# Performance work log

Measured on AMD Instinct MI355X. Metric: run time of the kernel, lower is better.

The kernel has to match this reference:

```python
import jax, jax.numpy as jnp
import numpy as np

C = 128
K = 7
RED = 4
C_RED = C // RED
PAD = (K - 1) // 2
BN_EPS = 1e-5


def setup_inputs() -> dict:
    key = jax.random.key(0)
    ks = jax.random.split(key, 7)
    b, h, w = 8, 56, 56
    x = jax.random.normal(ks[0], (b, C, h, w), dtype=jnp.float32)
    # 1x1 conv #1: c -> c_red
    w1 = jax.random.normal(ks[1], (C_RED, C), dtype=jnp.float32) * (1.0 / np.sqrt(C))
    b1 = jax.random.normal(ks[2], (C_RED,), dtype=jnp.float32) * 0.01
    # BatchNorm affine params
    gamma = jnp.ones((C_RED,), dtype=jnp.float32)
    beta = jnp.zeros((C_RED,), dtype=jnp.float32)
    # 1x1 conv #2: c_red -> k*k
    w2 = jax.random.normal(ks[3], (K * K, C_RED), dtype=jnp.float32) * (1.0 / np.sqrt(C_RED))
    b2 = jax.random.normal(ks[4], (K * K,), dtype=jnp.float32) * 0.01
    return {"x": x, "w1": w1, "b1": b1, "gamma": gamma, "beta": beta, "w2": w2, "b2": b2}


def _unfold(x):
    # torch.nn.Unfold(K, padding=PAD, stride=1) -> (b, c, k*k, h, w), channel-major
    b, c, h, w = x.shape
    xp = jnp.pad(x, ((0, 0), (0, 0), (PAD, PAD), (PAD, PAD)))
    patches = [xp[:, :, i:i + h, j:j + w] for i in range(K) for j in range(K)]
    return jnp.stack(patches, axis=2)  # (b, c, k*k, h, w)


def reference(x, w1, b1, gamma, beta, w2, b2):
    b, c, h, w = x.shape
    # kernel-generation branch: 1x1 conv -> BN (batch stats, training mode) -> ReLU -> 1x1 conv
    t = jnp.einsum('rc,bchw->brhw', w1, x) + b1[None, :, None, None]
    mean = t.mean(axis=(0, 2, 3))
    var = t.var(axis=(0, 2, 3))  # biased, as in torch BN normalization
    t = (t - mean[None, :, None, None]) * jax.lax.rsqrt(var + BN_EPS)[None, :, None, None]
    t = jax.nn.relu(t * gamma[None, :, None, None] + beta[None, :, None, None])
    kern = jnp.einsum('kr,brhw->bkhw', w2, t) + b2[None, :, None, None]  # (b, k*k, h, w)
    # involution: per-pixel kernel broadcast over channels, sum over k*k taps
    x_unf = _unfold(x)  # (b, c, k*k, h, w)
    return jnp.einsum('bkhw,bckhw->bchw', kern, x_unf)
```

## Files before the change

### kernel.cpp

```cpp
#include <hip/hip_runtime.h>

#define C 128
#define CRED 32
#define K 7
#define KK 49
#define H 56
#define W 56
#define P (H*W)
#define B 8
#define NPIX (B*P)
#define BN_EPS 1e-5

#define T_OFF 0
#define T_SIZE (B*CRED*P)
#define KERN_OFF (T_OFF + T_SIZE)
#define KERN_SIZE (B*KK*P)
#define NBLK_A (49*B)
#define PSUM_OFF (KERN_OFF + KERN_SIZE)
#define PSQ_OFF (PSUM_OFF + NBLK_A*CRED)
#define SS_OFF  (PSQ_OFF + NBLK_A*CRED)
#define SCALE_OFF SS_OFF
#define SHIFT_OFF (SS_OFF + CRED)
#define WS_NEED ((size_t)(SHIFT_OFF + CRED) * sizeof(float))

#define FB_SCALE_OFF T_SIZE
#define FB_SHIFT_OFF (T_SIZE + CRED)

__global__ __launch_bounds__(256) void kA_conv1(const float* __restrict__ x,
                                                const float* __restrict__ w1,
                                                const float* __restrict__ b1,
                                                float* __restrict__ ws) {
    __shared__ float s_w1t[C][16];
    int tid = threadIdx.x;
    int bx = blockIdx.x;
    int b  = blockIdx.y;
    int rh = blockIdx.z;
    for (int i = tid; i < C * 16; i += 256) {
        int c = i >> 4, rr = i & 15;
        s_w1t[c][rr] = w1[(rh * 16 + rr) * C + c];
    }
    __syncthreads();
    int px = tid & 63;
    int rq = tid >> 6;
    int p  = bx * 64 + px;
    int rbase = rh * 16 + rq * 4;
    const float* xb = x + (size_t)b * C * P + p;

    float a0 = 0.f, a1 = 0.f, a2 = 0.f, a3 = 0.f;
#pragma unroll 8
    for (int c = 0; c < C; ++c) {
        float xv = xb[(size_t)c * P];
        float4 wv = *(const float4*)&s_w1t[c][rq * 4];
        a0 = fmaf(wv.x, xv, a0);
        a1 = fmaf(wv.y, xv, a1);
        a2 = fmaf(wv.z, xv, a2);
        a3 = fmaf(wv.w, xv, a3);
    }
    a0 += b1[rbase + 0];
    a1 += b1[rbase + 1];
    a2 += b1[rbase + 2];
    a3 += b1[rbase + 3];

    float* tb = ws + T_OFF + (size_t)b * CRED * P + p;
    tb[(size_t)(rbase + 0) * P] = a0;
    tb[(size_t)(rbase + 1) * P] = a1;
    tb[(size_t)(rbase + 2) * P] = a2;
    tb[(size_t)(rbase + 3) * P] = a3;

    float s0 = a0, s1 = a1, s2 = a2, s3 = a3;
    float q0 = a0 * a0, q1 = a1 * a1, q2 = a2 * a2, q3 = a3 * a3;
#pragma unroll
    for (int off = 32; off; off >>= 1) {
        s0 += __shfl_xor(s0, off);  q0 += __shfl_xor(q0, off);
        s1 += __shfl_xor(s1, off);  q1 += __shfl_xor(q1, off);
        s2 += __shfl_xor(s2, off);  q2 += __shfl_xor(q2, off);
        s3 += __shfl_xor(s3, off);  q3 += __shfl_xor(q3, off);
    }
    if ((tid & 63) == 0) {
        int blk = b * 49 + bx;
        float* psum = ws + PSUM_OFF + (size_t)blk * CRED + rbase;
        float* psq  = ws + PSQ_OFF  + (size_t)blk * CRED + rbase;
        psum[0] = s0; psum[1] = s1; psum[2] = s2; psum[3] = s3;
        psq[0]  = q0; psq[1]  = q1; psq[2]  = q2; psq[3]  = q3;
    }
}

__global__ __launch_bounds__(256) void kB_bnfin(const float* __restrict__ gamma,
                                                const float* __restrict__ beta,
                                                float* __restrict__ ws) {
    __shared__ double sd1[8][CRED];
    __shared__ double sd2[8][CRED];
    int tid = threadIdx.x;
    int r = tid & 31, g = tid >> 5;
    double s1 = 0.0, s2 = 0.0;
    for (int i = g * 49; i < g * 49 + 49; ++i) {
        s1 += (double)ws[PSUM_OFF + i * CRED + r];
        s2 += (double)ws[PSQ_OFF + i * CRED + r];
    }
    sd1[g][r] = s1; sd2[g][r] = s2;
    __syncthreads();
    if (tid < CRED) {
        double S1 = 0.0, S2 = 0.0;
        for (int gg = 0; gg < 8; ++gg) { S1 += sd1[gg][tid]; S2 += sd2[gg][tid]; }
        double mean = S1 / NPIX;
        double var = S2 / NPIX - mean * mean;
        double sc = (double)gamma[tid] / sqrt(var + BN_EPS);
        ws[SCALE_OFF + tid] = (float)sc;
        ws[SHIFT_OFF + tid] = (float)((double)beta[tid] - mean * sc);
    }
}

__global__ __launch_bounds__(256) void kC_kern(const float* __restrict__ w2,
                                               const float* __restrict__ b2,
                                               float* __restrict__ ws) {
    __shared__ float s_t[CRED * W];
    __shared__ float s_w2[KK * CRED];
    int tid = threadIdx.x;
    int h = blockIdx.x, b = blockIdx.y;
    for (int i = tid; i < KK * CRED; i += 256) s_w2[i] = w2[i];
    const float* scale = ws + SCALE_OFF;
    const float* shift = ws + SHIFT_OFF;
    for (int i = tid; i < CRED * W; i += 256) {
        int r = i / W, w = i - r * W;
        float v = ws[T_OFF + ((size_t)b * CRED + r) * P + h * W + w];
        v = fmaf(v, scale[r], shift[r]);
        s_t[r * W + w] = fmaxf(v, 0.f);
    }
    __syncthreads();
    for (int i = tid; i < KK * W; i += 256) {
        int k = i / W, w = i - k * W;
        float acc = b2[k];
#pragma unroll
        for (int r = 0; r < CRED; ++r)
            acc = fmaf(s_w2[k * CRED + r], s_t[r * W + w], acc);
        ws[KERN_OFF + ((size_t)b * KK + k) * P + h * W + w] = acc;
    }
}

__global__ __launch_bounds__(256) void kD_inv(const float* __restrict__ x,
                                              const float* __restrict__ ws,
                                              float* __restrict__ out) {
    __shared__ float s_x0[10 * 64];
    __shared__ float s_x1[10 * 64];
    int tid = threadIdx.x;
    int hb = blockIdx.x;
    int z  = blockIdx.y;
    int b = hb / 14, ht = hb - b * 14;
    int h0 = ht * 4;
    int th = tid >> 6;
    int w  = tid & 63;
    int wl = min(w, W - 1);

    float kr[KK];
    {
        const float* kb = ws + KERN_OFF + (size_t)b * KK * P + (size_t)(h0 + th) * W + wl;
#pragma unroll
        for (int k = 0; k < KK; ++k) kr[k] = kb[(size_t)k * P];
    }

    int off0, off1, off2 = 0, v0, v1, v2 = 0;
    {
        int i = tid;
        int row = i >> 6, col = i & 63;
        int hh = h0 - 3 + row, ww = col - 3;
        v0 = ((unsigned)hh < H && (unsigned)ww < W);
        off0 = hh * W + ww;
        i = tid + 256;
        row = i >> 6; col = i & 63; hh = h0 - 3 + row; ww = col - 3;
        v1 = ((unsigned)hh < H && (unsigned)ww < W);
        off1 = hh * W + ww;
        i = tid + 512;
        if (i < 640) {
            row = i >> 6; col = i & 63; hh = h0 - 3 + row; ww = col - 3;
            v2 = ((unsigned)hh < H && (unsigned)ww < W);
            off2 = hh * W + ww;
        }
    }
    int cbase = z * 16;
    {
        const float* xc = x + ((size_t)b * C + cbase) * P;
        s_x0[tid]       = v0 ? xc[off0] : 0.f;
        s_x0[tid + 256] = v1 ? xc[off1] : 0.f;
        if (tid < 128) s_x0[tid + 512] = v2 ? xc[off2] : 0.f;
    }
#pragma unroll 2
    for (int cc = 0; cc < 16; ++cc) {
        __syncthreads();
        const float* s_cur = (cc & 1) ? s_x1 : s_x0;
        float* s_nxt = (cc & 1) ? s_x0 : s_x1;
        float n0 = 0.f, n1 = 0.f, n2 = 0.f;
        if (cc + 1 < 16) {
            const float* xc = x + ((size_t)b * C + cbase + cc + 1) * P;
            n0 = v0 ? xc[off0] : 0.f;
            n1 = v1 ? xc[off1] : 0.f;
            if (tid < 128) n2 = v2 ? xc[off2] : 0.f;
        }
        if (w < W) {
            const float* xs = s_cur + th * 64 + w;
            float acc = 0.f;
#pragma unroll
            for (int i = 0; i < K; ++i)
#pragma unroll
                for (int j = 0; j < K; ++j)
                    acc = fmaf(kr[i * 7 + j], xs[i * 64 + j], acc);
            out[((size_t)b * C + cbase + cc) * P + (size_t)(h0 + th) * W + w] = acc;
        }
        if (cc + 1 < 16) {
            s_nxt[tid]       = n0;
            s_nxt[tid + 256] = n1;
            if (tid < 128) s_nxt[tid + 512] = n2;
        }
    }
}

__global__ __launch_bounds__(256) void k1_conv1(const float* __restrict__ x,
                                                const float* __restrict__ w1,
                                                const float* __restrict__ b1,
                                                float* __restrict__ t) {
    __shared__ float s_w1t[C * CRED];
    int tid = threadIdx.x;
    for (int i = tid; i < C * CRED; i += 256) {
        int c = i >> 5, r = i & 31;
        s_w1t[i] = w1[r * C + c];
    }
    __syncthreads();
    int b = blockIdx.y;
    int p = blockIdx.x * 256 + tid;
    if (p >= P) return;
    float acc[CRED];
#pragma unroll
    for (int r = 0; r < CRED; ++r) acc[r] = 0.f;
    const float* xb = x + (size_t)b * C * P + p;
    for (int c = 0; c < C; ++c) {
        float xv = xb[(size_t)c * P];
#pragma unroll
        for (int r = 0; r < CRED; ++r)
            acc[r] = fmaf(s_w1t[c * CRED + r], xv, acc[r]);
    }
    float* tb = t + (size_t)b * CRED * P + p;
#pragma unroll
    for (int r = 0; r < CRED; ++r)
        tb[(size_t)r * P] = acc[r] + b1[r];
}

__global__ __launch_bounds__(256) void k2_bnstats(const float* __restrict__ t,
                                                  const float* __restrict__ gamma,
                                                  const float* __restrict__ beta,
                                                  float* __restrict__ scale,
                                                  float* __restrict__ shift) {
    int r = blockIdx.x;
    int tid = threadIdx.x;
    double s = 0.0, s2 = 0.0;
    for (int i = tid; i < NPIX; i += 256) {
        int b = i / P, p = i - b * P;
        float v = t[((size_t)b * CRED + r) * P + p];
        s += v;
        s2 += (double)v * v;
    }
    __shared__ double ls[256], ls2[256];
    ls[tid] = s; ls2[tid] = s2;
    __syncthreads();
    for (int off = 128; off > 0; off >>= 1) {
        if (tid < off) { ls[tid] += ls[tid + off]; ls2[tid] += ls2[tid + off]; }
        __syncthreads();
    }
    if (tid == 0) {
        double mean = ls[0] / NPIX;
        double var = ls2[0] / NPIX - mean * mean;
        double sc = (double)gamma[r] / sqrt(var + BN_EPS);
        scale[r] = (float)sc;
        shift[r] = (float)((double)beta[r] - mean * sc);
    }
}

__global__ __launch_bounds__(256) void k3_involution(const float* __restrict__ x,
                                                     const float* __restrict__ t,
                                                     const float* __restrict__ scale,
                                                     const float* __restrict__ shift,
                                                     const float* __restrict__ w2,
                                                     const float* __restrict__ b2,
                                                     float* __restrict__ out) {
    int h = blockIdx.x;
    int b = blockIdx.y;
    int z = blockIdx.z;
    int tid = threadIdx.x;
    __shared__ float s_w2[KK * CRED];
    __shared__ float s_t[CRED * W];
    __shared__ float s_kern[KK][W];
    __shared__ float s_x[4][K][64];
    for (int i = tid; i < KK * CRED; i += 256) s_w2[i] = w2[i];
    for (int i = tid; i < CRED * W; i += 256) {
        int r = i / W, w = i - r * W;
        float v = t[((size_t)b * CRED + r) * P + h * W + w];
        v = fmaf(v, scale[r], shift[r]);
        s_t[r * W + w] = fmaxf(v, 0.f);
    }
    __syncthreads();
    for (int i = tid; i < KK * W; i += 256) {
        int k = i / W, w = i - k * W;
        float acc = b2[k];
#pragma unroll
        for (int r = 0; r < CRED; ++r)
            acc = fmaf(s_w2[k * CRED + r], s_t[r * W + w], acc);
        s_kern[k][w] = acc;
    }
    __syncthreads();
    int w = tid % W;
    int c4 = tid / W;
    float kr[KK];
#pragma unroll
    for (int k = 0; k < KK; ++k) kr[k] = s_kern[k][w];
    int cbase = z * (C / 2);
    for (int cg = cbase; cg < cbase + C / 2; cg += 4) {
        for (int i = tid; i < 4 * K * 64; i += 256) {
            int col = i & 63;
            int rc = i >> 6;
            int cc = rc / K;
            int row = rc - cc * K;
            int hh = h - 3 + row;
            int ww = col - 3;
            float v = 0.f;
            if ((unsigned)hh < H && (unsigned)ww < W)
                v = x[(((size_t)b * C + cg + cc) * H + hh) * W + ww];
            s_x[cc][row][col] = v;
        }
        __syncthreads();
        if (tid < 4 * W) {
            float acc = 0.f;
#pragma unroll
            for (int i = 0; i < K; ++i)
#pragma unroll
                for (int j = 0; j < K; ++j)
                    acc = fmaf(kr[i * K + j], s_x[c4][i][w + j], acc);
            out[(((size_t)b * C + cg + c4) * H + h) * W + w] = acc;
        }
        __syncthreads();
    }
}

extern "C" void kernel_launch(void* const* d_in, const int* in_sizes, int n_in,
                              void* d_out, int out_size, void* d_ws, size_t ws_size,
                              hipStream_t stream) {
    const float* x     = (const float*)d_in[0];
    const float* w1    = (const float*)d_in[1];
    const float* b1    = (const float*)d_in[2];
    const float* gamma = (const float*)d_in[3];
    const float* beta  = (const float*)d_in[4];
    const float* w2    = (const float*)d_in[5];
    const float* b2    = (const float*)d_in[6];
    float* out = (float*)d_out;
    float* ws  = (float*)d_ws;

    if (ws_size >= WS_NEED) {
        dim3 gA(49, B, 2);
        kA_conv1<<<gA, 256, 0, stream>>>(x, w1, b1, ws);
        kB_bnfin<<<1, 256, 0, stream>>>(gamma, beta, ws);
        dim3 gC(H, B);
        kC_kern<<<gC, 256, 0, stream>>>(w2, b2, ws);
        dim3 gD(112, 8);
        kD_inv<<<gD, 256, 0, stream>>>(x, ws, out);
    } else {
        float* t     = ws;
        float* scale = ws + FB_SCALE_OFF;
        float* shift = ws + FB_SHIFT_OFF;
        dim3 g1((P + 255) / 256, B);
        k1_conv1<<<g1, 256, 0, stream>>>(x, w1, b1, t);
        k2_bnstats<<<CRED, 256, 0, stream>>>(t, gamma, beta, scale, shift);
        dim3 g3(H, B, 2);
        k3_involution<<<g3, 256, 0, stream>>>(x, t, scale, shift, w2, b2, out);
    }
}
```

Baseline: 52.95 us.

## Restructure conv1, kernel-gen and involution kernels for more data reuse

The first conv now computes all 32 reduced channels per block, reading weights through scalar loads. This removes the shared-memory transpose and the duplicate read of x across two channel halves. The kernel-generation step computes four pixels per thread using vectorized shared loads and a padded weight layout. The involution kernel uses taller 8-row tiles with 448 threads and stores four channels interleaved as float4 in shared memory, cutting halo overhead and shared loads per FMA. The trade-off is higher register pressure and more shared memory per block.

```diff
diff --git a/kernel.cpp b/kernel.cpp
--- a/kernel.cpp
+++ b/kernel.cpp
@@ -30,58 +30,50 @@
                                                 const float* __restrict__ w1,
                                                 const float* __restrict__ b1,
                                                 float* __restrict__ ws) {
-    __shared__ float s_w1t[C][16];
     int tid = threadIdx.x;
     int bx = blockIdx.x;
     int b  = blockIdx.y;
-    int rh = blockIdx.z;
-    for (int i = tid; i < C * 16; i += 256) {
-        int c = i >> 4, rr = i & 15;
-        s_w1t[c][rr] = w1[(rh * 16 + rr) * C + c];
-    }
-    __syncthreads();
     int px = tid & 63;
-    int rq = tid >> 6;
     int p  = bx * 64 + px;
-    int rbase = rh * 16 + rq * 4;
+    int ru8 = __builtin_amdgcn_readfirstlane((tid >> 6) * 8);
+    const float* __restrict__ wq = w1 + (size_t)ru8 * C;
     const float* xb = x + (size_t)b * C * P + p;
 
-    float a0 = 0.f, a1 = 0.f, a2 = 0.f, a3 = 0.f;
+    float acc[8];
+#pragma unroll
+    for (int u = 0; u < 8; ++u) acc[u] = 0.f;
 #pragma unroll 8
     for (int c = 0; c < C; ++c) {
         float xv = xb[(size_t)c * P];
-        float4 wv = *(const float4*)&s_w1t[c][rq * 4];
-        a0 = fmaf(wv.x, xv, a0);
-        a1 = fmaf(wv.y, xv, a1);
-        a2 = fmaf(wv.z, xv, a2);
-        a3 = fmaf(wv.w, xv, a3);
-    }
-    a0 += b1[rbase + 0];
-    a1 += b1[rbase + 1];
-    a2 += b1[rbase + 2];
-    a3 += b1[rbase + 3];
+#pragma unroll
+        for (int u = 0; u < 8; ++u)
+            acc[u] = fmaf(wq[u * C + c], xv, acc[u]);
+    }
+#pragma unroll
+    for (int u = 0; u < 8; ++u) acc[u] += b1[ru8 + u];
 
     float* tb = ws + T_OFF + (size_t)b * CRED * P + p;
-    tb[(size_t)(rbase + 0) * P] = a0;
-    tb[(size_t)(rbase + 1) * P] = a1;
-    tb[(size_t)(rbase + 2) * P] = a2;
-    tb[(size_t)(rbase + 3) * P] = a3;
-
-    float s0 = a0, s1 = a1, s2 = a2, s3 = a3;
-    float q0 = a0 * a0, q1 = a1 * a1, q2 = a2 * a2, q3 = a3 * a3;
+#pragma unroll
+    for (int u = 0; u < 8; ++u)
+        tb[(size_t)(ru8 + u) * P] = acc[u];
+
+    float s[8], q[8];
+#pragma unroll
+    for (int u = 0; u < 8; ++u) { s[u] = acc[u]; q[u] = acc[u] * acc[u]; }
 #pragma unroll
     for (int off = 32; off; off >>= 1) {
-        s0 += __shfl_xor(s0, off);  q0 += __shfl_xor(q0, off);
-        s1 += __shfl_xor(s1, off);  q1 += __shfl_xor(q1, off);
-        s2 += __shfl_xor(s2, off);  q2 += __shfl_xor(q2, off);
-        s3 += __shfl_xor(s3, off);  q3 += __shfl_xor(q3, off);
-    }
-    if ((tid & 63) == 0) {
+#pragma unroll
+        for (int u = 0; u < 8; ++u) {
+            s[u] += __shfl_xor(s[u], off);
+            q[u] += __shfl_xor(q[u], off);
+        }
+    }
+    if (px == 0) {
         int blk = b * 49 + bx;
-        float* psum = ws + PSUM_OFF + (size_t)blk * CRED + rbase;
-        float* psq  = ws + PSQ_OFF  + (size_t)blk * CRED + rbase;
-        psum[0] = s0; psum[1] = s1; psum[2] = s2; psum[3] = s3;
-        psq[0]  = q0; psq[1]  = q1; psq[2]  = q2; psq[3]  = q3;
+        float* psum = ws + PSUM_OFF + (size_t)blk * CRED + ru8;
+        float* psq  = ws + PSQ_OFF  + (size_t)blk * CRED + ru8;
+#pragma unroll
+        for (int u = 0; u < 8; ++u) { psum[u] = s[u]; psq[u] = q[u]; }
     }
 }
 
@@ -114,10 +106,13 @@
                                                const float* __restrict__ b2,
                                                float* __restrict__ ws) {
     __shared__ float s_t[CRED * W];
-    __shared__ float s_w2[KK * CRED];
+    __shared__ float s_w2[KK * 33];
     int tid = threadIdx.x;
     int h = blockIdx.x, b = blockIdx.y;
-    for (int i = tid; i < KK * CRED; i += 256) s_w2[i] = w2[i];
+    for (int i = tid; i < KK * CRED; i += 256) {
+        int k = i >> 5, r = i & 31;
+        s_w2[k * 33 + r] = w2[i];
+    }
     const float* scale = ws + SCALE_OFF;
     const float* shift = ws + SHIFT_OFF;
     for (int i = tid; i < CRED * W; i += 256) {
@@ -127,88 +122,109 @@
         s_t[r * W + w] = fmaxf(v, 0.f);
     }
     __syncthreads();
-    for (int i = tid; i < KK * W; i += 256) {
-        int k = i / W, w = i - k * W;
-        float acc = b2[k];
-#pragma unroll
-        for (int r = 0; r < CRED; ++r)
-            acc = fmaf(s_w2[k * CRED + r], s_t[r * W + w], acc);
-        ws[KERN_OFF + ((size_t)b * KK + k) * P + h * W + w] = acc;
-    }
-}
-
-__global__ __launch_bounds__(256) void kD_inv(const float* __restrict__ x,
+    for (int i = tid; i < KK * 14; i += 256) {
+        int k = i / 14, w0 = (i - k * 14) * 4;
+        float bb = b2[k];
+        float a0 = bb, a1 = bb, a2 = bb, a3 = bb;
+#pragma unroll
+        for (int r = 0; r < CRED; ++r) {
+            float4 tv = *(const float4*)&s_t[r * W + w0];
+            float wv = s_w2[k * 33 + r];
+            a0 = fmaf(wv, tv.x, a0);
+            a1 = fmaf(wv, tv.y, a1);
+            a2 = fmaf(wv, tv.z, a2);
+            a3 = fmaf(wv, tv.w, a3);
+        }
+        float4 o = {a0, a1, a2, a3};
+        *(float4*)&ws[KERN_OFF + ((size_t)b * KK + k) * P + h * W + w0] = o;
+    }
+}
+
+#define TH 8
+#define XROWS 14
+#define XPITCH 68
+__global__ __launch_bounds__(448) void kD_inv(const float* __restrict__ x,
                                               const float* __restrict__ ws,
                                               float* __restrict__ out) {
-    __shared__ float s_x0[10 * 64];
-    __shared__ float s_x1[10 * 64];
-    int tid = threadIdx.x;
-    int hb = blockIdx.x;
+    __shared__ float4 s_x[2][XROWS * XPITCH];
+    int tid = threadIdx.x;
+    int bx = blockIdx.x;
     int z  = blockIdx.y;
-    int b = hb / 14, ht = hb - b * 14;
-    int h0 = ht * 4;
-    int th = tid >> 6;
-    int w  = tid & 63;
-    int wl = min(w, W - 1);
+    int b = bx / 7, ht = bx - b * 7;
+    int h0 = ht * TH;
+    int orow = tid / W;
+    int ocol = tid - orow * W;
+    int sbase = orow * XPITCH + ocol;
 
     float kr[KK];
     {
-        const float* kb = ws + KERN_OFF + (size_t)b * KK * P + (size_t)(h0 + th) * W + wl;
+        const float* kb = ws + KERN_OFF + (size_t)b * KK * P + (size_t)h0 * W + tid;
 #pragma unroll
         for (int k = 0; k < KK; ++k) kr[k] = kb[(size_t)k * P];
     }
 
-    int off0, off1, off2 = 0, v0, v1, v2 = 0;
+    int slot0, slot1, off0, off1, v0, v1;
     {
-        int i = tid;
-        int row = i >> 6, col = i & 63;
+        int q = tid;
+        int row = q >> 6, col = q & 63;
         int hh = h0 - 3 + row, ww = col - 3;
         v0 = ((unsigned)hh < H && (unsigned)ww < W);
         off0 = hh * W + ww;
-        i = tid + 256;
-        row = i >> 6; col = i & 63; hh = h0 - 3 + row; ww = col - 3;
+        slot0 = row * XPITCH + col;
+        q = tid + 448;
+        row = q >> 6; col = q & 63;
+        hh = h0 - 3 + row; ww = col - 3;
         v1 = ((unsigned)hh < H && (unsigned)ww < W);
         off1 = hh * W + ww;
-        i = tid + 512;
-        if (i < 640) {
-            row = i >> 6; col = i & 63; hh = h0 - 3 + row; ww = col - 3;
-            v2 = ((unsigned)hh < H && (unsigned)ww < W);
-            off2 = hh * W + ww;
-        }
-    }
-    int cbase = z * 16;
+        slot1 = row * XPITCH + col;
+    }
+
+    int cg0 = z * 16;
+    const size_t xbase = ((size_t)b * C + cg0) * P;
     {
-        const float* xc = x + ((size_t)b * C + cbase) * P;
-        s_x0[tid]       = v0 ? xc[off0] : 0.f;
-        s_x0[tid + 256] = v1 ? xc[off1] : 0.f;
-        if (tid < 128) s_x0[tid + 512] = v2 ? xc[off2] : 0.f;
-    }
-#pragma unroll 2
-    for (int cc = 0; cc < 16; ++cc) {
+        const float* xc = x + xbase;
+        float4 f0, f1;
+        f0.x = v0 ? xc[off0] : 0.f;  f0.y = v0 ? xc[P + off0] : 0.f;
+        f0.z = v0 ? xc[2 * P + off0] : 0.f;  f0.w = v0 ? xc[3 * P + off0] : 0.f;
+        f1.x = v1 ? xc[off1] : 0.f;  f1.y = v1 ? xc[P + off1] : 0.f;
+        f1.z = v1 ? xc[2 * P + off1] : 0.f;  f1.w = v1 ? xc[3 * P + off1] : 0.f;
+        s_x[0][slot0] = f0;
+        s_x[0][slot1] = f1;
+    }
+
+    for (int it = 0; it < 4; ++it) {
         __syncthreads();
-        const float* s_cur = (cc & 1) ? s_x1 : s_x0;
-        float* s_nxt = (cc & 1) ? s_x0 : s_x1;
-        float n0 = 0.f, n1 = 0.f, n2 = 0.f;
-        if (cc + 1 < 16) {
-            const float* xc = x + ((size_t)b * C + cbase + cc + 1) * P;
-            n0 = v0 ? xc[off0] : 0.f;
-            n1 = v1 ? xc[off1] : 0.f;
-            if (tid < 128) n2 = v2 ? xc[off2] : 0.f;
-        }
-        if (w < W) {
-            const float* xs = s_cur + th * 64 + w;
-            float acc = 0.f;
-#pragma unroll
-            for (int i = 0; i < K; ++i)
-#pragma unroll
-                for (int j = 0; j < K; ++j)
-                    acc = fmaf(kr[i * 7 + j], xs[i * 64 + j], acc);
-            out[((size_t)b * C + cbase + cc) * P + (size_t)(h0 + th) * W + w] = acc;
-        }
-        if (cc + 1 < 16) {
-            s_nxt[tid]       = n0;
-            s_nxt[tid + 256] = n1;
-            if (tid < 128) s_nxt[tid + 512] = n2;
+        float4 n0, n1;
+        if (it < 3) {
+            const float* xc = x + xbase + (size_t)(it + 1) * 4 * P;
+            n0.x = v0 ? xc[off0] : 0.f;  n0.y = v0 ? xc[P + off0] : 0.f;
+            n0.z = v0 ? xc[2 * P + off0] : 0.f;  n0.w = v0 ? xc[3 * P + off0] : 0.f;
+            n1.x = v1 ? xc[off1] : 0.f;  n1.y = v1 ? xc[P + off1] : 0.f;
+            n1.z = v1 ? xc[2 * P + off1] : 0.f;  n1.w = v1 ? xc[3 * P + off1] : 0.f;
+        }
+        const float4* xs = s_x[it & 1] + sbase;
+        float a0 = 0.f, a1 = 0.f, a2 = 0.f, a3 = 0.f;
+#pragma unroll
+        for (int i = 0; i < K; ++i) {
+#pragma unroll
+            for (int j = 0; j < K; ++j) {
+                float4 xv = xs[i * XPITCH + j];
+                float kv = kr[i * 7 + j];
+                a0 = fmaf(kv, xv.x, a0);
+                a1 = fmaf(kv, xv.y, a1);
+                a2 = fmaf(kv, xv.z, a2);
+                a3 = fmaf(kv, xv.w, a3);
+            }
+        }
+        float* ob = out + xbase + (size_t)it * 4 * P + (size_t)h0 * W + tid;
+        ob[0]     = a0;
+        ob[P]     = a1;
+        ob[2 * P] = a2;
+        ob[3 * P] = a3;
+        if (it < 3) {
+            float4* nb = s_x[(it + 1) & 1];
+            nb[slot0] = n0;
+            nb[slot1] = n1;
         }
     }
 }
@@ -352,13 +368,13 @@
     float* ws  = (float*)d_ws;
 
     if (ws_size >= WS_NEED) {
-        dim3 gA(49, B, 2);
+        dim3 gA(49, B);
         kA_conv1<<<gA, 256, 0, stream>>>(x, w1, b1, ws);
         kB_bnfin<<<1, 256, 0, stream>>>(gamma, beta, ws);
         dim3 gC(H, B);
         kC_kern<<<gC, 256, 0, stream>>>(w2, b2, ws);
-        dim3 gD(112, 8);
-        kD_inv<<<gD, 256, 0, stream>>>(x, ws, out);
+        dim3 gD(7 * B, 8);
+        kD_inv<<<gD, 448, 0, stream>>>(x, ws, out);
     } else {
         float* t     = ws;
         float* scale = ws + FB_SCALE_OFF;
```

Result: faster. 44.42 us (-16.1%).
